# Optimization experiments

Hardware: AMD Instinct MI355X
Metric: run time of the kernel (lower is better)

## Reference

```python
import jax, jax.numpy as jnp
import numpy as np

N_NODES = 10000
N_EDGES = 320000
D = 128  # feature dim for edges, nodes, globals


def setup_inputs() -> dict:
    key = jax.random.key(0)
    ks = jax.random.split(key, 8)
    edges = jax.random.normal(ks[0], (N_EDGES, D), dtype=jnp.float32)
    nodes = jax.random.normal(ks[1], (N_NODES, D), dtype=jnp.float32)
    globals_ = jax.random.normal(ks[2], (D,), dtype=jnp.float32)
    receivers = jax.random.randint(ks[3], (N_EDGES,), 0, N_NODES, dtype=jnp.int32).astype(jnp.int64)
    senders = jax.random.randint(ks[4], (N_EDGES,), 0, N_NODES, dtype=jnp.int32).astype(jnp.int64)
    W1 = jax.random.normal(ks[5], (4 * D, 256), dtype=jnp.float32) * (1.0 / np.sqrt(4 * D))
    b1 = jnp.zeros((256,), dtype=jnp.float32)
    W2 = jax.random.normal(ks[6], (256, D), dtype=jnp.float32) * (1.0 / np.sqrt(256))
    b2 = jnp.zeros((D,), dtype=jnp.float32)
    return {"edges": edges, "nodes": nodes, "globals_": globals_,
            "receivers": receivers, "senders": senders,
            "W1": W1, "b1": b1, "W2": W2, "b2": b2}


def reference(edges, nodes, globals_, receivers, senders, W1, b1, W2, b2):
    # Gather adjacent node features to edges, broadcast globals, concat.
    recv_feats = nodes[receivers]                 # [E, D]
    send_feats = nodes[senders]                   # [E, D]
    glob_feats = jnp.broadcast_to(globals_, (edges.shape[0], globals_.shape[0]))  # [E, D]
    x = jnp.concatenate([edges, recv_feats, send_feats, glob_feats], axis=-1)     # [E, 4D]
    # Edge-update MLP: 4D -> 256 -> D with relu.
    h = jax.nn.relu(x @ W1 + b1)
    new_edges = h @ W2 + b2                       # [E, D]
    return new_edges
```

## Files before the change

kernel.cpp:

```cpp
#include <hip/hip_runtime.h>
#include <hip/hip_bf16.h>

#define D 128
#define NH 256
#define BM 64
#define E_TOTAL 320000
#define NNODES 10000

typedef __attribute__((ext_vector_type(8))) short bf16x8;
typedef __attribute__((ext_vector_type(4))) float f32x4;

__device__ __forceinline__ unsigned short f2b(float f) {
  unsigned int u = __builtin_bit_cast(unsigned int, f);
  u += 0x7fffu + ((u >> 16) & 1u);
  return (unsigned short)(u >> 16);
}
__device__ __forceinline__ unsigned pk2(float a, float b) {
  return (unsigned)f2b(a) | ((unsigned)f2b(b) << 16);
}
__device__ __forceinline__ uint4 pack8(float4 a, float4 b) {
  uint4 r;
  r.x = pk2(a.x, a.y); r.y = pk2(a.z, a.w);
  r.z = pk2(b.x, b.y); r.w = pk2(b.z, b.w);
  return r;
}
__device__ __forceinline__ float lo2f(unsigned u) {
  return __builtin_bit_cast(float, u << 16);
}
__device__ __forceinline__ float hi2f(unsigned u) {
  return __builtin_bit_cast(float, u & 0xffff0000u);
}
__device__ __forceinline__ void gload16(const void* g, void* l) {
  __builtin_amdgcn_global_load_lds(
      (const __attribute__((address_space(1))) void*)g,
      (__attribute__((address_space(3))) void*)l, 16, 0, 0);
}
__device__ __forceinline__ void barrier_lgkm() {
  asm volatile("s_waitcnt lgkmcnt(0)" ::: "memory");
  __builtin_amdgcn_sched_barrier(0);
  __builtin_amdgcn_s_barrier();
  __builtin_amdgcn_sched_barrier(0);
}
__device__ __forceinline__ void barrier_vm0() {
  asm volatile("s_waitcnt vmcnt(0) lgkmcnt(0)" ::: "memory");
  __builtin_amdgcn_sched_barrier(0);
  __builtin_amdgcn_s_barrier();
  __builtin_amdgcn_sched_barrier(0);
}

__global__ __launch_bounds__(512, 4) void prep_nodeh_kernel(
    const float* __restrict__ nodes,
    const float* __restrict__ W1,
    const float* __restrict__ W2,
    const float* __restrict__ b1,
    const float* __restrict__ g,
    ushort* __restrict__ W1pk,
    ushort* __restrict__ W2p,
    float* __restrict__ cvec,
    ushort* __restrict__ tblR,
    ushort* __restrict__ tblS) {
  __shared__ char Xn[BM * 256];
  const int b = blockIdx.x;
  const int tid = threadIdx.x;

  if (b < 24) {
    int c = b * 512 + tid;
    int s = c >> 12;
    int rem = c & 4095;
    int nt = rem >> 8;
    int rem2 = rem & 255;
    int ks = rem2 >> 6;
    int l = rem2 & 63;
    int col = nt * 16 + (l & 15);
    int k0 = s * 128 + ks * 32 + (l >> 4) * 8;
    ushort* dst = W1pk + (size_t)c * 8;
    #pragma unroll
    for (int j = 0; j < 8; ++j)
      dst[j] = f2b(W1[(size_t)(k0 + j) * NH + col]);
    return;
  }
  if (b < 32) {
    int c = (b - 24) * 512 + tid;
    int nt2 = c / (8 * 64);
    int rem = c % (8 * 64);
    int ks = rem >> 6;
    int l = rem & 63;
    int col = nt2 * 16 + (l & 15);
    int k0 = ks * 32 + (l >> 4) * 8;
    ushort* dst = W2p + (size_t)c * 8;
    #pragma unroll
    for (int j = 0; j < 8; ++j)
      dst[j] = f2b(W2[(size_t)(k0 + j) * D + col]);
    return;
  }
  if (b == 32) {
    if (tid < 256) {
      int n = tid;
      float acc = b1[n];
      for (int k = 0; k < D; ++k)
        acc += g[k] * W1[(size_t)(384 + k) * NH + n];
      cvec[n] = acc;
    }
    return;
  }

  const int bi = b - 33;
  const int role = bi >= 157;
  ushort* __restrict__ tbl = role ? tblS : tblR;
  const int nb = (bi - role * 157) * BM;

  {
    int row = tid >> 4;
    int cc = (tid & 15) * 16;
    #pragma unroll
    for (int q = 0; q < 2; ++q) {
      int r = row + q * 32;
      int rg = nb + r; if (rg >= NNODES) rg = NNODES - 1;
      const float* np = nodes + (size_t)rg * D + (tid & 15) * 8;
      float4 u0 = *(const float4*)np;
      float4 u1 = *(const float4*)(np + 4);
      *(uint4*)(Xn + r * 256 + (cc ^ ((r & 7) << 4))) = pack8(u0, u1);
    }
  }
  __syncthreads();

  const int lane = tid & 63;
  const int wave = tid >> 6;
  const int lr = lane & 15;
  const int kg = lane >> 4;
  const int col = wave * 32 + lr;

  bf16x8 aw[4][2];
  #pragma unroll
  for (int ks = 0; ks < 4; ++ks)
    #pragma unroll
    for (int ht = 0; ht < 2; ++ht) {
      int k0 = (1 + role) * 128 + ks * 32 + kg * 8;
      bf16x8 fr;
      #pragma unroll
      for (int j = 0; j < 8; ++j)
        fr[j] = (short)f2b(W1[(size_t)(k0 + j) * NH + col + ht * 16]);
      aw[ks][ht] = fr;
    }

  f32x4 acc[2][4] = {};
  #pragma unroll
  for (int ks = 0; ks < 4; ++ks) {
    const int k0 = ks * 32 + kg * 8;
    bf16x8 xb[4];
    #pragma unroll
    for (int et = 0; et < 4; ++et) {
      int row = et * 16 + lr;
      xb[et] = *(const bf16x8*)(Xn + row * 256 + ((k0 * 2) ^ ((row & 7) << 4)));
    }
    #pragma unroll
    for (int ht = 0; ht < 2; ++ht)
      #pragma unroll
      for (int et = 0; et < 4; ++et)
        acc[ht][et] = __builtin_amdgcn_mfma_f32_16x16x32_bf16(aw[ks][ht], xb[et], acc[ht][et], 0, 0, 0);
  }

  #pragma unroll
  for (int ht = 0; ht < 2; ++ht) {
    int h0 = wave * 32 + ht * 16 + kg * 4;
    #pragma unroll
    for (int et = 0; et < 4; ++et) {
      int n = nb + et * 16 + lr;
      if (n < NNODES) {
        uint2 pk;
        pk.x = pk2(acc[ht][et][0], acc[ht][et][1]);
        pk.y = pk2(acc[ht][et][2], acc[ht][et][3]);
        *(uint2*)(tbl + (size_t)n * NH + h0) = pk;
      }
    }
  }
}

__global__ __launch_bounds__(512, 4) void fused_kernel(
    const float* __restrict__ edges,
    const int* __restrict__ receivers,
    const int* __restrict__ senders,
    const ushort* __restrict__ W1pk,
    const ushort* __restrict__ tblR,
    const ushort* __restrict__ tblS,
    const float* __restrict__ cvec,
    const ushort* __restrict__ W2p,
    const float* __restrict__ b2,
    float* __restrict__ out) {
  __shared__ char Xs[BM * 256];
  __shared__ char Hr[BM * 512];
  __shared__ char Hsb[BM * 512];

  const int ebase = blockIdx.x * BM;
  const int tid = threadIdx.x;
  const int lane = tid & 63;
  const int wave = tid >> 6;
  const int lr = lane & 15;
  const int kg = lane >> 4;

  const int wslice = wave & 3;
  const int isS = wave >> 2;
  const int* __restrict__ myarr = isS ? senders : receivers;
  const char* mytbl = (const char*)(isS ? tblS : tblR);
  char* myLds = isS ? Hsb : Hr;
  const int half = lane >> 5;
  const int ch16 = (lane & 31) * 16;
  int idx[8];
  #pragma unroll
  for (int j = 0; j < 8; ++j)
    idx[j] = myarr[ebase + wslice * 16 + 2 * j + half];

  const ushort* w1base = W1pk + (size_t)(wave * 2) * 2048 + lane * 8;
  bf16x8 aw[4][2];
  #pragma unroll
  for (int ks = 0; ks < 4; ++ks)
    #pragma unroll
    for (int ht = 0; ht < 2; ++ht)
      aw[ks][ht] = *(const bf16x8*)(w1base + ht * 2048 + ks * 512);

  float4 cva = *(const float4*)(cvec + wave * 32 + kg * 4);
  float4 cvb = *(const float4*)(cvec + wave * 32 + 16 + kg * 4);

  const int erow = tid >> 4;
  const int ecc = (tid & 15) * 16;
  const float* ep0 = edges + (size_t)(ebase + erow) * D + (tid & 15) * 8;
  float4 e0 = *(const float4*)ep0;
  float4 e1 = *(const float4*)(ep0 + 4);
  const float* ep1 = edges + (size_t)(ebase + erow + 32) * D + (tid & 15) * 8;
  float4 e2 = *(const float4*)ep1;
  float4 e3 = *(const float4*)(ep1 + 4);

  #pragma unroll
  for (int j = 0; j < 8; ++j) {
    int r = wslice * 16 + 2 * j + half;
    gload16(mytbl + (size_t)idx[j] * 512 + (ch16 ^ ((r & 7) << 4)),
            myLds + (wslice * 16 + 2 * j) * 512);
  }

  *(uint4*)(Xs + erow * 256 + (ecc ^ ((erow & 7) << 4))) = pack8(e0, e1);
  {
    int r2 = erow + 32;
    *(uint4*)(Xs + r2 * 256 + (ecc ^ ((r2 & 7) << 4))) = pack8(e2, e3);
  }

  barrier_lgkm();

  f32x4 acc[2][4] = {};
  #pragma unroll
  for (int ks = 0; ks < 4; ++ks) {
    const int k0 = ks * 32 + kg * 8;
    bf16x8 xb[4];
    #pragma unroll
    for (int et = 0; et < 4; ++et) {
      int row = et * 16 + lr;
      xb[et] = *(const bf16x8*)(Xs + row * 256 + ((k0 * 2) ^ ((row & 7) << 4)));
    }
    #pragma unroll
    for (int ht = 0; ht < 2; ++ht)
      #pragma unroll
      for (int et = 0; et < 4; ++et)
        acc[ht][et] = __builtin_amdgcn_mfma_f32_16x16x32_bf16(aw[ks][ht], xb[et], acc[ht][et], 0, 0, 0);
  }

  barrier_vm0();

  const int wm3 = wave >> 1;
  const int wn3 = wave & 1;
  const ushort* w2base = W2p + (size_t)(wm3 * 2) * 8 * 512 + lane * 8;
  bf16x8 aw2[2][2];
  #pragma unroll
  for (int mt = 0; mt < 2; ++mt)
    aw2[0][mt] = *(const bf16x8*)(w2base + (size_t)mt * 8 * 512);

  const int h0 = wave * 32 + kg * 4;
  #pragma unroll
  for (int ht = 0; ht < 2; ++ht) {
    const float4 cvq = ht ? cvb : cva;
    const int h0b = (h0 + ht * 16) * 2;
    #pragma unroll
    for (int et = 0; et < 4; ++et) {
      int e = et * 16 + lr;
      int ad = e * 512 + (h0b ^ ((e & 7) << 4));
      uint2 gr = *(uint2*)(Hr + ad);
      uint2 gs = *(uint2*)(Hsb + ad);
      float v0 = acc[ht][et][0] + cvq.x + lo2f(gr.x) + lo2f(gs.x);
      float v1 = acc[ht][et][1] + cvq.y + hi2f(gr.x) + hi2f(gs.x);
      float v2 = acc[ht][et][2] + cvq.z + lo2f(gr.y) + lo2f(gs.y);
      float v3 = acc[ht][et][3] + cvq.w + hi2f(gr.y) + hi2f(gs.y);
      v0 = v0 > 0.f ? v0 : 0.f;
      v1 = v1 > 0.f ? v1 : 0.f;
      v2 = v2 > 0.f ? v2 : 0.f;
      v3 = v3 > 0.f ? v3 : 0.f;
      uint2 pk;
      pk.x = pk2(v0, v1);
      pk.y = pk2(v2, v3);
      *(uint2*)(Hr + ad) = pk;
    }
  }

  barrier_lgkm();

  float4 ba = *(const float4*)(b2 + wm3 * 32 + kg * 4);
  float4 bb2 = *(const float4*)(b2 + wm3 * 32 + 16 + kg * 4);
  f32x4 acc2[2][2] = {};
  #pragma unroll
  for (int ks = 0; ks < 8; ++ks) {
    const int cur = ks & 1, nxt = cur ^ 1;
    if (ks < 7) {
      #pragma unroll
      for (int mt = 0; mt < 2; ++mt)
        aw2[nxt][mt] = *(const bf16x8*)(w2base + (size_t)mt * 8 * 512 + (ks + 1) * 512);
    }
    const int k0 = ks * 32 + kg * 8;
    bf16x8 hb[2];
    #pragma unroll
    for (int et2 = 0; et2 < 2; ++et2) {
      int e = wn3 * 32 + et2 * 16 + lr;
      hb[et2] = *(const bf16x8*)(Hr + e * 512 + ((k0 * 2) ^ ((e & 7) << 4)));
    }
    #pragma unroll
    for (int mt = 0; mt < 2; ++mt)
      #pragma unroll
      for (int et2 = 0; et2 < 2; ++et2)
        acc2[mt][et2] = __builtin_amdgcn_mfma_f32_16x16x32_bf16(aw2[cur][mt], hb[et2], acc2[mt][et2], 0, 0, 0);
  }

  #pragma unroll
  for (int mt = 0; mt < 2; ++mt) {
    const float4 bq = mt ? bb2 : ba;
    const int c0 = wm3 * 32 + mt * 16 + kg * 4;
    #pragma unroll
    for (int et2 = 0; et2 < 2; ++et2) {
      int e = wn3 * 32 + et2 * 16 + lr;
      float4 o;
      o.x = acc2[mt][et2][0] + bq.x;
      o.y = acc2[mt][et2][1] + bq.y;
      o.z = acc2[mt][et2][2] + bq.z;
      o.w = acc2[mt][et2][3] + bq.w;
      *(float4*)(out + (size_t)(ebase + e) * D + c0) = o;
    }
  }
}

extern "C" void kernel_launch(void* const* d_in, const int* in_sizes, int n_in,
                              void* d_out, int out_size, void* d_ws, size_t ws_size,
                              hipStream_t stream) {
  const float* edges     = (const float*)d_in[0];
  const float* nodes     = (const float*)d_in[1];
  const float* globals_  = (const float*)d_in[2];
  const int*   receivers = (const int*)d_in[3];
  const int*   senders   = (const int*)d_in[4];
  const float* W1        = (const float*)d_in[5];
  const float* b1        = (const float*)d_in[6];
  const float* W2        = (const float*)d_in[7];
  const float* b2        = (const float*)d_in[8];
  float* out = (float*)d_out;

  char* ws = (char*)d_ws;
  ushort* W1pk = (ushort*)ws;
  ushort* W2p  = (ushort*)(ws + 196608);
  float*  cvec = (float*)(ws + 262144);
  ushort* tblR = (ushort*)(ws + 263168);
  ushort* tblS = (ushort*)(ws + 5383168);

  hipLaunchKernelGGL(prep_nodeh_kernel, dim3(33 + 314), dim3(512), 0, stream,
                     nodes, W1, W2, b1, globals_, W1pk, W2p, cvec, tblR, tblS);
  hipLaunchKernelGGL(fused_kernel, dim3(E_TOTAL / BM), dim3(512), 0, stream,
                     edges, receivers, senders, W1pk, tblR, tblS, cvec, W2p, b2, out);
}
```

Before: 145.3 us.

## Make fused edge kernel persistent with double-buffered gather prefetch

Replaces the one-block-per-tile launch of 5000 blocks with 256 persistent blocks that loop over edge tiles. The next tile's node-table gathers go into a second LDS buffer and its edge rows into registers while the current tile's MLP runs, and indices are prefetched two tiles ahead. The goal is to hide gather and load latency behind MFMA work. The cost is lower occupancy: more LDS per block, the occupancy hint dropped from launch bounds, and only 256 blocks, which may underfill the GPU's compute units.

Result: faster. 142.1 us (-2.2%).

```diff
diff --git a/kernel.cpp b/kernel.cpp
--- a/kernel.cpp
+++ b/kernel.cpp
@@ -5,6 +5,8 @@
 #define NH 256
 #define BM 64
 #define E_TOTAL 320000
+#define NTILES 5000
+#define NBLK 256
 #define NNODES 10000
 
 typedef __attribute__((ext_vector_type(8))) short bf16x8;
@@ -176,7 +178,7 @@
   }
 }
 
-__global__ __launch_bounds__(512, 4) void fused_kernel(
+__global__ __launch_bounds__(512) void fused_kernel(
     const float* __restrict__ edges,
     const int* __restrict__ receivers,
     const int* __restrict__ senders,
@@ -187,11 +189,10 @@
     const ushort* __restrict__ W2p,
     const float* __restrict__ b2,
     float* __restrict__ out) {
-  __shared__ char Xs[BM * 256];
-  __shared__ char Hr[BM * 512];
-  __shared__ char Hsb[BM * 512];
-
-  const int ebase = blockIdx.x * BM;
+  __shared__ char Xe[BM * 256];
+  __shared__ char Hr[2][BM * 512];
+  __shared__ char Hsb[2][BM * 512];
+
   const int tid = threadIdx.x;
   const int lane = tid & 63;
   const int wave = tid >> 6;
@@ -202,143 +203,192 @@
   const int isS = wave >> 2;
   const int* __restrict__ myarr = isS ? senders : receivers;
   const char* mytbl = (const char*)(isS ? tblS : tblR);
-  char* myLds = isS ? Hsb : Hr;
   const int half = lane >> 5;
   const int ch16 = (lane & 31) * 16;
-  int idx[8];
-  #pragma unroll
-  for (int j = 0; j < 8; ++j)
-    idx[j] = myarr[ebase + wslice * 16 + 2 * j + half];
-
-  const ushort* w1base = W1pk + (size_t)(wave * 2) * 2048 + lane * 8;
-  bf16x8 aw[4][2];
-  #pragma unroll
-  for (int ks = 0; ks < 4; ++ks)
-    #pragma unroll
-    for (int ht = 0; ht < 2; ++ht)
-      aw[ks][ht] = *(const bf16x8*)(w1base + ht * 2048 + ks * 512);
-
-  float4 cva = *(const float4*)(cvec + wave * 32 + kg * 4);
-  float4 cvb = *(const float4*)(cvec + wave * 32 + 16 + kg * 4);
 
   const int erow = tid >> 4;
   const int ecc = (tid & 15) * 16;
-  const float* ep0 = edges + (size_t)(ebase + erow) * D + (tid & 15) * 8;
-  float4 e0 = *(const float4*)ep0;
-  float4 e1 = *(const float4*)(ep0 + 4);
-  const float* ep1 = edges + (size_t)(ebase + erow + 32) * D + (tid & 15) * 8;
-  float4 e2 = *(const float4*)ep1;
-  float4 e3 = *(const float4*)(ep1 + 4);
-
-  #pragma unroll
-  for (int j = 0; j < 8; ++j) {
-    int r = wslice * 16 + 2 * j + half;
-    gload16(mytbl + (size_t)idx[j] * 512 + (ch16 ^ ((r & 7) << 4)),
-            myLds + (wslice * 16 + 2 * j) * 512);
-  }
-
-  *(uint4*)(Xs + erow * 256 + (ecc ^ ((erow & 7) << 4))) = pack8(e0, e1);
-  {
-    int r2 = erow + 32;
-    *(uint4*)(Xs + r2 * 256 + (ecc ^ ((r2 & 7) << 4))) = pack8(e2, e3);
-  }
-
-  barrier_lgkm();
-
-  f32x4 acc[2][4] = {};
-  #pragma unroll
-  for (int ks = 0; ks < 4; ++ks) {
-    const int k0 = ks * 32 + kg * 8;
-    bf16x8 xb[4];
-    #pragma unroll
-    for (int et = 0; et < 4; ++et) {
-      int row = et * 16 + lr;
-      xb[et] = *(const bf16x8*)(Xs + row * 256 + ((k0 * 2) ^ ((row & 7) << 4)));
-    }
-    #pragma unroll
-    for (int ht = 0; ht < 2; ++ht)
-      #pragma unroll
-      for (int et = 0; et < 4; ++et)
-        acc[ht][et] = __builtin_amdgcn_mfma_f32_16x16x32_bf16(aw[ks][ht], xb[et], acc[ht][et], 0, 0, 0);
-  }
-
-  barrier_vm0();
-
+
+  const float4 cva = *(const float4*)(cvec + wave * 32 + kg * 4);
+  const float4 cvb = *(const float4*)(cvec + wave * 32 + 16 + kg * 4);
   const int wm3 = wave >> 1;
   const int wn3 = wave & 1;
+  const ushort* w1base = W1pk + (size_t)(wave * 2) * 2048 + lane * 8;
   const ushort* w2base = W2p + (size_t)(wm3 * 2) * 8 * 512 + lane * 8;
-  bf16x8 aw2[2][2];
-  #pragma unroll
-  for (int mt = 0; mt < 2; ++mt)
-    aw2[0][mt] = *(const bf16x8*)(w2base + (size_t)mt * 8 * 512);
-
-  const int h0 = wave * 32 + kg * 4;
-  #pragma unroll
-  for (int ht = 0; ht < 2; ++ht) {
-    const float4 cvq = ht ? cvb : cva;
-    const int h0b = (h0 + ht * 16) * 2;
-    #pragma unroll
-    for (int et = 0; et < 4; ++et) {
-      int e = et * 16 + lr;
-      int ad = e * 512 + (h0b ^ ((e & 7) << 4));
-      uint2 gr = *(uint2*)(Hr + ad);
-      uint2 gs = *(uint2*)(Hsb + ad);
-      float v0 = acc[ht][et][0] + cvq.x + lo2f(gr.x) + lo2f(gs.x);
-      float v1 = acc[ht][et][1] + cvq.y + hi2f(gr.x) + hi2f(gs.x);
-      float v2 = acc[ht][et][2] + cvq.z + lo2f(gr.y) + lo2f(gs.y);
-      float v3 = acc[ht][et][3] + cvq.w + hi2f(gr.y) + hi2f(gs.y);
-      v0 = v0 > 0.f ? v0 : 0.f;
-      v1 = v1 > 0.f ? v1 : 0.f;
-      v2 = v2 > 0.f ? v2 : 0.f;
-      v3 = v3 > 0.f ? v3 : 0.f;
-      uint2 pk;
-      pk.x = pk2(v0, v1);
-      pk.y = pk2(v2, v3);
-      *(uint2*)(Hr + ad) = pk;
-    }
-  }
-
-  barrier_lgkm();
-
-  float4 ba = *(const float4*)(b2 + wm3 * 32 + kg * 4);
-  float4 bb2 = *(const float4*)(b2 + wm3 * 32 + 16 + kg * 4);
-  f32x4 acc2[2][2] = {};
-  #pragma unroll
-  for (int ks = 0; ks < 8; ++ks) {
-    const int cur = ks & 1, nxt = cur ^ 1;
-    if (ks < 7) {
+  const float4 ba   = *(const float4*)(b2 + wm3 * 32 + kg * 4);
+  const float4 bb2v = *(const float4*)(b2 + wm3 * 32 + 16 + kg * 4);
+
+  int t = blockIdx.x;
+  int idxn[8];
+
+  {
+    char* myLds0 = (isS ? Hsb[0] : Hr[0]);
+    #pragma unroll
+    for (int j = 0; j < 8; ++j) {
+      int r = wslice * 16 + 2 * j + half;
+      int id0 = myarr[(size_t)t * BM + r];
+      gload16(mytbl + (size_t)id0 * 512 + (ch16 ^ ((r & 7) << 4)),
+              myLds0 + (wslice * 16 + 2 * j) * 512);
+    }
+    const float* ep0 = edges + (size_t)(t * BM + erow) * D + (tid & 15) * 8;
+    float4 e0 = *(const float4*)ep0;
+    float4 e1 = *(const float4*)(ep0 + 4);
+    const float* ep1 = edges + (size_t)(t * BM + erow + 32) * D + (tid & 15) * 8;
+    float4 e2 = *(const float4*)ep1;
+    float4 e3 = *(const float4*)(ep1 + 4);
+    *(uint4*)(Xe + erow * 256 + (ecc ^ ((erow & 7) << 4))) = pack8(e0, e1);
+    int r2 = erow + 32;
+    *(uint4*)(Xe + r2 * 256 + (ecc ^ ((r2 & 7) << 4))) = pack8(e2, e3);
+    int tn0 = (t + NBLK < NTILES) ? t + NBLK : t;
+    #pragma unroll
+    for (int j = 0; j < 8; ++j)
+      idxn[j] = myarr[(size_t)tn0 * BM + wslice * 16 + 2 * j + half];
+  }
+  barrier_vm0();
+
+  int cur = 0;
+  for (; t < NTILES; t += NBLK) {
+    const int nxt = cur ^ 1;
+    const int tn = (t + NBLK < NTILES) ? t + NBLK : t;
+    const int t2 = (t + 2 * NBLK < NTILES) ? t + 2 * NBLK : tn;
+    const int eb = t * BM;
+
+    {
+      char* myLdsN = (isS ? Hsb[nxt] : Hr[nxt]);
+      #pragma unroll
+      for (int j = 0; j < 8; ++j) {
+        int r = wslice * 16 + 2 * j + half;
+        gload16(mytbl + (size_t)idxn[j] * 512 + (ch16 ^ ((r & 7) << 4)),
+                myLdsN + (wslice * 16 + 2 * j) * 512);
+      }
+    }
+
+    float4 ev0, ev1, ev2, ev3;
+    {
+      const float* ep0 = edges + (size_t)(tn * BM + erow) * D + (tid & 15) * 8;
+      ev0 = *(const float4*)ep0;
+      ev1 = *(const float4*)(ep0 + 4);
+      const float* ep1 = edges + (size_t)(tn * BM + erow + 32) * D + (tid & 15) * 8;
+      ev2 = *(const float4*)ep1;
+      ev3 = *(const float4*)(ep1 + 4);
+    }
+
+    int idx2[8];
+    #pragma unroll
+    for (int j = 0; j < 8; ++j)
+      idx2[j] = myarr[(size_t)t2 * BM + wslice * 16 + 2 * j + half];
+
+    f32x4 acc[2][4] = {};
+    {
+      bf16x8 aw[2][2];
+      #pragma unroll
+      for (int ht = 0; ht < 2; ++ht)
+        aw[0][ht] = *(const bf16x8*)(w1base + ht * 2048);
+      #pragma unroll
+      for (int ks = 0; ks < 4; ++ks) {
+        if (ks < 3) {
+          #pragma unroll
+          for (int ht = 0; ht < 2; ++ht)
+            aw[(ks + 1) & 1][ht] = *(const bf16x8*)(w1base + ht * 2048 + (ks + 1) * 512);
+        }
+        const int k0 = ks * 32 + kg * 8;
+        bf16x8 xb[4];
+        #pragma unroll
+        for (int et = 0; et < 4; ++et) {
+          int row = et * 16 + lr;
+          xb[et] = *(const bf16x8*)(Xe + row * 256 + ((k0 * 2) ^ ((row & 7) << 4)));
+        }
+        #pragma unroll
+        for (int ht = 0; ht < 2; ++ht)
+          #pragma unroll
+          for (int et = 0; et < 4; ++et)
+            acc[ht][et] = __builtin_amdgcn_mfma_f32_16x16x32_bf16(aw[ks & 1][ht], xb[et], acc[ht][et], 0, 0, 0);
+      }
+    }
+
+    bf16x8 aw2[2][2];
+    #pragma unroll
+    for (int mt = 0; mt < 2; ++mt)
+      aw2[0][mt] = *(const bf16x8*)(w2base + (size_t)mt * 8 * 512);
+
+    const int h0 = wave * 32 + kg * 4;
+    #pragma unroll
+    for (int ht = 0; ht < 2; ++ht) {
+      const float4 cvq = ht ? cvb : cva;
+      const int h0b = (h0 + ht * 16) * 2;
+      #pragma unroll
+      for (int et = 0; et < 4; ++et) {
+        int e = et * 16 + lr;
+        int ad = e * 512 + (h0b ^ ((e & 7) << 4));
+        uint2 gr = *(uint2*)(Hr[cur] + ad);
+        uint2 gs = *(uint2*)(Hsb[cur] + ad);
+        float v0 = acc[ht][et][0] + cvq.x + lo2f(gr.x) + lo2f(gs.x);
+        float v1 = acc[ht][et][1] + cvq.y + hi2f(gr.x) + hi2f(gs.x);
+        float v2 = acc[ht][et][2] + cvq.z + lo2f(gr.y) + lo2f(gs.y);
+        float v3 = acc[ht][et][3] + cvq.w + hi2f(gr.y) + hi2f(gs.y);
+        v0 = v0 > 0.f ? v0 : 0.f;
+        v1 = v1 > 0.f ? v1 : 0.f;
+        v2 = v2 > 0.f ? v2 : 0.f;
+        v3 = v3 > 0.f ? v3 : 0.f;
+        uint2 pk;
+        pk.x = pk2(v0, v1);
+        pk.y = pk2(v2, v3);
+        *(uint2*)(Hr[cur] + ad) = pk;
+      }
+    }
+
+    barrier_lgkm();
+
+    f32x4 acc2[2][2] = {};
+    #pragma unroll
+    for (int ks = 0; ks < 8; ++ks) {
+      const int c2 = ks & 1, nx2 = c2 ^ 1;
+      if (ks < 7) {
+        #pragma unroll
+        for (int mt = 0; mt < 2; ++mt)
+          aw2[nx2][mt] = *(const bf16x8*)(w2base + (size_t)mt * 8 * 512 + (ks + 1) * 512);
+      }
+      const int k0 = ks * 32 + kg * 8;
+      bf16x8 hb[2];
+      #pragma unroll
+      for (int et2 = 0; et2 < 2; ++et2) {
+        int e = wn3 * 32 + et2 * 16 + lr;
+        hb[et2] = *(const bf16x8*)(Hr[cur] + e * 512 + ((k0 * 2) ^ ((e & 7) << 4)));
+      }
       #pragma unroll
       for (int mt = 0; mt < 2; ++mt)
-        aw2[nxt][mt] = *(const bf16x8*)(w2base + (size_t)mt * 8 * 512 + (ks + 1) * 512);
-    }
-    const int k0 = ks * 32 + kg * 8;
-    bf16x8 hb[2];
-    #pragma unroll
-    for (int et2 = 0; et2 < 2; ++et2) {
-      int e = wn3 * 32 + et2 * 16 + lr;
-      hb[et2] = *(const bf16x8*)(Hr + e * 512 + ((k0 * 2) ^ ((e & 7) << 4)));
-    }
-    #pragma unroll
-    for (int mt = 0; mt < 2; ++mt)
-      #pragma unroll
-      for (int et2 = 0; et2 < 2; ++et2)
-        acc2[mt][et2] = __builtin_amdgcn_mfma_f32_16x16x32_bf16(aw2[cur][mt], hb[et2], acc2[mt][et2], 0, 0, 0);
-  }
-
-  #pragma unroll
-  for (int mt = 0; mt < 2; ++mt) {
-    const float4 bq = mt ? bb2 : ba;
-    const int c0 = wm3 * 32 + mt * 16 + kg * 4;
-    #pragma unroll
-    for (int et2 = 0; et2 < 2; ++et2) {
-      int e = wn3 * 32 + et2 * 16 + lr;
-      float4 o;
-      o.x = acc2[mt][et2][0] + bq.x;
-      o.y = acc2[mt][et2][1] + bq.y;
-      o.z = acc2[mt][et2][2] + bq.z;
-      o.w = acc2[mt][et2][3] + bq.w;
-      *(float4*)(out + (size_t)(ebase + e) * D + c0) = o;
-    }
+        #pragma unroll
+        for (int et2 = 0; et2 < 2; ++et2)
+          acc2[mt][et2] = __builtin_amdgcn_mfma_f32_16x16x32_bf16(aw2[c2][mt], hb[et2], acc2[mt][et2], 0, 0, 0);
+    }
+
+    #pragma unroll
+    for (int mt = 0; mt < 2; ++mt) {
+      const float4 bq = mt ? bb2v : ba;
+      const int c0 = wm3 * 32 + mt * 16 + kg * 4;
+      #pragma unroll
+      for (int et2 = 0; et2 < 2; ++et2) {
+        int e = wn3 * 32 + et2 * 16 + lr;
+        float4 o;
+        o.x = acc2[mt][et2][0] + bq.x;
+        o.y = acc2[mt][et2][1] + bq.y;
+        o.z = acc2[mt][et2][2] + bq.z;
+        o.w = acc2[mt][et2][3] + bq.w;
+        *(float4*)(out + (size_t)(eb + e) * D + c0) = o;
+      }
+    }
+
+    *(uint4*)(Xe + erow * 256 + (ecc ^ ((erow & 7) << 4))) = pack8(ev0, ev1);
+    {
+      int r2 = erow + 32;
+      *(uint4*)(Xe + r2 * 256 + (ecc ^ ((r2 & 7) << 4))) = pack8(ev2, ev3);
+    }
+
+    #pragma unroll
+    for (int j = 0; j < 8; ++j) idxn[j] = idx2[j];
+
+    barrier_vm0();
+    cur = nxt;
   }
 }
 
@@ -365,6 +415,6 @@
 
   hipLaunchKernelGGL(prep_nodeh_kernel, dim3(33 + 314), dim3(512), 0, stream,
                      nodes, W1, W2, b1, globals_, W1pk, W2p, cvec, tblR, tblS);
-  hipLaunchKernelGGL(fused_kernel, dim3(E_TOTAL / BM), dim3(512), 0, stream,
+  hipLaunchKernelGGL(fused_kernel, dim3(NBLK), dim3(512), 0, stream,
                      edges, receivers, senders, W1pk, tblR, tblS, cvec, W2p, b2, out);
 }
```
